# Optimization experiments

Measured on AMD Instinct MI355X. Metric: run time of the kernel, lower is better.

## Reference

```python
import jax, jax.numpy as jnp
import numpy as np

D_MODEL = 768
D_LAT = 384
N_FREQ = D_MODEL // 2 + 1  # 385
INIT_S = 0.02


def _quat_linear(x, Ww, Wx, Wy, Wz, b):
    # Ww..Wz: [out_q, in_q]; x: [..., 4*in_q]
    d = Ww.shape[1]
    xw, xx, xy, xz = x[..., :d], x[..., d:2*d], x[..., 2*d:3*d], x[..., 3*d:]
    lin = lambda W, v: jnp.einsum('...i,oi->...o', v, W)
    ow = lin(Ww, xw) - lin(Wx, xx) - lin(Wy, xy) - lin(Wz, xz)
    ox = lin(Ww, xx) + lin(Wx, xw) + lin(Wy, xz) - lin(Wz, xy)
    oy = lin(Ww, xy) - lin(Wx, xz) + lin(Wy, xw) + lin(Wz, xx)
    oz = lin(Ww, xz) + lin(Wx, xy) - lin(Wy, xx) + lin(Wz, xw)
    return jnp.concatenate([ow, ox, oy, oz], axis=-1) + b


def _filter1d(x, kr, ki, n):
    X = jnp.fft.rfft(x, axis=-1)
    K = kr + 1j * ki
    return jnp.fft.irfft(X * K, n=n, axis=-1)


def setup_inputs() -> dict:
    key = jax.random.key(0)
    ks = jax.random.split(key, 16)
    rn = lambda k, shape: jax.random.normal(k, shape, dtype=jnp.float32)
    in_q_e, out_q_e = D_MODEL // 4, D_LAT // 4   # 192, 96
    in_q_d, out_q_d = D_LAT // 4, D_MODEL // 4   # 96, 192
    return {
        'x': rn(ks[0], (8, 4096, D_MODEL)),
        'enc_kr': rn(ks[1], (N_FREQ,)) * INIT_S,
        'enc_ki': rn(ks[2], (N_FREQ,)) * INIT_S,
        'dec_kr': rn(ks[3], (N_FREQ,)) * INIT_S,
        'dec_ki': rn(ks[4], (N_FREQ,)) * INIT_S,
        'enc_Ww': rn(ks[5], (out_q_e, in_q_e)) * 0.02,
        'enc_Wx': rn(ks[6], (out_q_e, in_q_e)) * 0.02,
        'enc_Wy': rn(ks[7], (out_q_e, in_q_e)) * 0.02,
        'enc_Wz': rn(ks[8], (out_q_e, in_q_e)) * 0.02,
        'enc_b': jnp.zeros((D_LAT,), jnp.float32),
        'dec_Ww': rn(ks[9], (out_q_d, in_q_d)) * 0.02,
        'dec_Wx': rn(ks[10], (out_q_d, in_q_d)) * 0.02,
        'dec_Wy': rn(ks[11], (out_q_d, in_q_d)) * 0.02,
        'dec_Wz': rn(ks[12], (out_q_d, in_q_d)) * 0.02,
        'dec_b': jnp.zeros((D_MODEL,), jnp.float32),
    }


def reference(x, enc_kr, enc_ki, dec_kr, dec_ki,
              enc_Ww, enc_Wx, enc_Wy, enc_Wz, enc_b,
              dec_Ww, dec_Wx, dec_Wy, dec_Wz, dec_b):
    # encode: spectral filter -> GELU (exact erf, matching nn.GELU) -> quaternion proj
    h = jax.nn.gelu(_filter1d(x, enc_kr, enc_ki, D_MODEL), approximate=False)
    z = _quat_linear(h, enc_Ww, enc_Wx, enc_Wy, enc_Wz, enc_b)
    # decode: quaternion proj -> spectral filter
    recon = _filter1d(_quat_linear(z, dec_Ww, dec_Wx, dec_Wy, dec_Wz, dec_b),
                      dec_kr, dec_ki, D_MODEL)
    loss = jnp.mean((recon - jax.lax.stop_gradient(x)) ** 2)
    return z, loss
```

## Files before the change

kernel.cpp:

```cpp
#include <hip/hip_runtime.h>
#include <hip/hip_bf16.h>
#include <math.h>

typedef unsigned short u16;
typedef __attribute__((ext_vector_type(8))) short s8v;
typedef __attribute__((ext_vector_type(4))) float f4v;

#define DM 768
#define DL 384

__device__ __forceinline__ u16 f2bf(float f) {
  union { float f; unsigned u; } v; v.f = f;
  unsigned r = v.u + 0x7fffu + ((v.u >> 16) & 1u);
  return (u16)(r >> 16);
}
__device__ __forceinline__ float bf2f(u16 b) {
  union { unsigned u; float f; } v; v.u = ((unsigned)b) << 16; return v.f;
}

__global__ void k_build_c2(const float* __restrict__ kr0, const float* __restrict__ ki0,
                           const float* __restrict__ kr1, const float* __restrict__ ki1,
                           float* __restrict__ c0, float* __restrict__ c1) {
  const float* kr = blockIdx.y ? kr1 : kr0;
  const float* ki = blockIdx.y ? ki1 : ki0;
  float* c = blockIdx.y ? c1 : c0;
  const int t = blockIdx.x;
  const int f = threadIdx.x;
  float s = 0.f;
  for (int ff = f; ff < 384; ff += 256) {
    if (ff >= 1) {
      int ph = (ff * t) % DM;
      float th = (float)ph * (6.283185307179586f / DM);
      float sn, cs; sincosf(th, &sn, &cs);
      s += 2.f * (kr[ff] * cs - ki[ff] * sn);
    }
  }
  if (f == 0) s += kr[0] + ((t & 1) ? -kr[384] : kr[384]);
  __shared__ float red[256];
  red[f] = s; __syncthreads();
  for (int k = 128; k > 0; k >>= 1) {
    if (f < k) red[f] += red[f + k];
    __syncthreads();
  }
  if (f == 0) c[t] = red[0] * (1.f / DM);
}

__global__ void k_rb2(const float* __restrict__ c, const float* __restrict__ b,
                      float* __restrict__ rb) {
  const int i = blockIdx.x;
  const int f = threadIdx.x;
  float s = 0.f;
  for (int j = f; j < DM; j += 256) {
    int ci = i - j; if (ci < 0) ci += DM;
    s += c[ci] * b[j];
  }
  __shared__ float red[256];
  red[f] = s; __syncthreads();
  for (int k = 128; k > 0; k >>= 1) {
    if (f < k) red[f] += red[f + k];
    __syncthreads();
  }
  if (f == 0) rb[i] = red[0];
}

__global__ void k_circ(const float* __restrict__ c, u16* __restrict__ B) {
  int idx = blockIdx.x * 256 + threadIdx.x;
  int i = idx / DM, j = idx % DM;
  int d = i - j; if (d < 0) d += DM;
  B[idx] = f2bf(c[d]);
}

__device__ __constant__ int   MI_[4][4] = {{0,1,2,3},{1,0,3,2},{2,3,0,1},{3,2,1,0}};
__device__ __constant__ float SG_[4][4] = {{1,-1,-1,-1},{1,1,-1,1},{1,1,1,-1},{1,-1,1,1}};

__global__ void k_wenc(const float* __restrict__ Ww, const float* __restrict__ Wx,
                       const float* __restrict__ Wy, const float* __restrict__ Wz,
                       u16* __restrict__ B) {
  int idx = blockIdx.x * 256 + threadIdx.x;
  int o = idx / DM, j = idx % DM;
  int p = o / 96, r = o % 96, q = j / 192, cc = j % 192;
  const float* Ws[4] = {Ww, Wx, Wy, Wz};
  B[idx] = f2bf(SG_[p][q] * Ws[MI_[p][q]][r * 192 + cc]);
}

__global__ void k_ddecT(const float* __restrict__ Ww, const float* __restrict__ Wx,
                        const float* __restrict__ Wy, const float* __restrict__ Wz,
                        u16* __restrict__ B) {
  int idx = blockIdx.x * 256 + threadIdx.x;
  int o = idx / DM, j = idx % DM;
  int p = j / 192, r = j % 192, q = o / 96, cc = o % 96;
  const float* Ws[4] = {Ww, Wx, Wy, Wz};
  B[idx] = f2bf(SG_[p][q] * Ws[MI_[p][q]][r * 96 + cc]);
}

__global__ void k_cvt(const float4* __restrict__ x, u16* __restrict__ xb) {
  int i = blockIdx.x * 256 + threadIdx.x;
  float4 v = x[i];
  union { u16 u[4]; unsigned long long q; } o;
  o.u[0] = f2bf(v.x); o.u[1] = f2bf(v.y); o.u[2] = f2bf(v.z); o.u[3] = f2bf(v.w);
  *(unsigned long long*)(xb + (size_t)i * 4) = o.q;
}

__device__ __forceinline__ void ld_lds16(const u16* g, u16* l) {
  __builtin_amdgcn_global_load_lds((const __attribute__((address_space(1))) void*)g,
                                   (__attribute__((address_space(3))) void*)l, 16, 0, 0);
}

template <int KT, int EPI>
__global__ __launch_bounds__(512, 1) void gemm8(
    const u16* __restrict__ A, const u16* __restrict__ B,
    u16* __restrict__ outb, const float* __restrict__ bias,
    const float* __restrict__ xref, float* __restrict__ partials) {
  __shared__ __align__(16) u16 SM[65536];
  const int t = threadIdx.x;
  const int lane = t & 63, wid = t >> 6;
  const int wrow = wid >> 2, wcol = wid & 3;
  int wg = blockIdx.x;
  { const int q = gridDim.x >> 3; wg = (wg & 7) * q + (wg >> 3); }
  const int bm = wg / 3, bn = wg % 3;
  constexpr int NKT = KT / 64;

  f4v acc[8][4];
#pragma unroll
  for (int m = 0; m < 8; ++m)
#pragma unroll
    for (int n = 0; n < 4; ++n) acc[m][n] = (f4v)0.f;

  const int srow = t >> 3;
  const int sgrp = (t & 7) ^ (srow & 7);
  const u16* gA = A + (size_t)(bm * 256 + srow) * KT + sgrp * 8;
  const u16* gB = B + (size_t)(bn * 256 + srow) * KT + sgrp * 8;
  const int sx = ((lane >> 4) ^ (lane & 7)) * 8;
  const int ABASE = wrow * 8192 + (lane & 15) * 64;
  const int BBASE = 32768 + (wcol >> 1) * 8192 + (wcol & 1) * 4096 + (lane & 15) * 64;

  auto stg = [&](int opd, int kt_, int half_) {
    const u16* g = (opd ? gB : gA) + (size_t)(half_ * 128) * KT + kt_ * 64;
    u16* l = SM + opd * 32768 + (kt_ & 1) * 16384 + half_ * 8192 + t * 8;
    ld_lds16(g, l);
    ld_lds16(g + 64 * KT, l + 4096);
  };

  stg(0, 0, 0); stg(1, 0, 0); stg(0, 0, 1); stg(1, 0, 1); stg(0, 1, 0); stg(1, 1, 0);
  asm volatile("s_waitcnt vmcnt(4)" ::: "memory");
  __builtin_amdgcn_sched_barrier(0);
  __builtin_amdgcn_s_barrier();

  s8v a0[4][2], a1[4][2], b0[2][2], b1[2][2];
#pragma unroll
  for (int kt = 0; kt < NKT; ++kt) {
    const int cb = (kt & 1) * 16384;
#pragma unroll
    for (int m = 0; m < 4; ++m) {
      a0[m][0] = *(const s8v*)(SM + cb + ABASE + m * 1024 + sx);
      a0[m][1] = *(const s8v*)(SM + cb + ABASE + m * 1024 + (sx ^ 32));
    }
#pragma unroll
    for (int n = 0; n < 2; ++n) {
      b0[n][0] = *(const s8v*)(SM + cb + BBASE + n * 1024 + sx);
      b0[n][1] = *(const s8v*)(SM + cb + BBASE + n * 1024 + (sx ^ 32));
    }
    if (kt + 1 < NKT) stg(0, kt + 1, 1);
    __builtin_amdgcn_s_barrier();
    asm volatile("s_waitcnt lgkmcnt(0)" ::: "memory");
    __builtin_amdgcn_sched_barrier(0);
    __builtin_amdgcn_s_setprio(1);
#pragma unroll
    for (int m = 0; m < 4; ++m)
#pragma unroll
      for (int n = 0; n < 2; ++n) {
        acc[m][n] = __builtin_amdgcn_mfma_f32_16x16x32_bf16(a0[m][0], b0[n][0], acc[m][n], 0, 0, 0);
        acc[m][n] = __builtin_amdgcn_mfma_f32_16x16x32_bf16(a0[m][1], b0[n][1], acc[m][n], 0, 0, 0);
      }
    __builtin_amdgcn_s_setprio(0);
    __builtin_amdgcn_s_barrier();
#pragma unroll
    for (int m = 0; m < 4; ++m) {
      a1[m][0] = *(const s8v*)(SM + cb + ABASE + (4 + m) * 1024 + sx);
      a1[m][1] = *(const s8v*)(SM + cb + ABASE + (4 + m) * 1024 + (sx ^ 32));
    }
    if (kt + 1 < NKT) stg(1, kt + 1, 1);
    __builtin_amdgcn_s_barrier();
    asm volatile("s_waitcnt lgkmcnt(0)" ::: "memory");
    __builtin_amdgcn_sched_barrier(0);
    __builtin_amdgcn_s_setprio(1);
#pragma unroll
    for (int m = 0; m < 4; ++m)
#pragma unroll
      for (int n = 0; n < 2; ++n) {
        acc[4 + m][n] = __builtin_amdgcn_mfma_f32_16x16x32_bf16(a1[m][0], b0[n][0], acc[4 + m][n], 0, 0, 0);
        acc[4 + m][n] = __builtin_amdgcn_mfma_f32_16x16x32_bf16(a1[m][1], b0[n][1], acc[4 + m][n], 0, 0, 0);
      }
    __builtin_amdgcn_s_setprio(0);
    __builtin_amdgcn_s_barrier();
#pragma unroll
    for (int n = 0; n < 2; ++n) {
      b1[n][0] = *(const s8v*)(SM + cb + BBASE + (2 + n) * 1024 + sx);
      b1[n][1] = *(const s8v*)(SM + cb + BBASE + (2 + n) * 1024 + (sx ^ 32));
    }
    if (kt + 2 < NKT) stg(0, kt + 2, 0);
    __builtin_amdgcn_s_barrier();
    asm volatile("s_waitcnt lgkmcnt(0)" ::: "memory");
    __builtin_amdgcn_sched_barrier(0);
    __builtin_amdgcn_s_setprio(1);
#pragma unroll
    for (int m = 0; m < 4; ++m)
#pragma unroll
      for (int n = 0; n < 2; ++n) {
        acc[4 + m][2 + n] = __builtin_amdgcn_mfma_f32_16x16x32_bf16(a1[m][0], b1[n][0], acc[4 + m][2 + n], 0, 0, 0);
        acc[4 + m][2 + n] = __builtin_amdgcn_mfma_f32_16x16x32_bf16(a1[m][1], b1[n][1], acc[4 + m][2 + n], 0, 0, 0);
      }
    __builtin_amdgcn_s_setprio(0);
    __builtin_amdgcn_s_barrier();
    if (kt + 2 < NKT) {
      stg(1, kt + 2, 0);
      asm volatile("s_waitcnt vmcnt(4)" ::: "memory");
    } else {
      asm volatile("s_waitcnt vmcnt(0)" ::: "memory");
    }
    __builtin_amdgcn_sched_barrier(0);
    __builtin_amdgcn_s_barrier();
    __builtin_amdgcn_s_setprio(1);
#pragma unroll
    for (int m = 0; m < 4; ++m)
#pragma unroll
      for (int n = 0; n < 2; ++n) {
        acc[m][2 + n] = __builtin_amdgcn_mfma_f32_16x16x32_bf16(a0[m][0], b1[n][0], acc[m][2 + n], 0, 0, 0);
        acc[m][2 + n] = __builtin_amdgcn_mfma_f32_16x16x32_bf16(a0[m][1], b1[n][1], acc[m][2 + n], 0, 0, 0);
      }
    __builtin_amdgcn_s_setprio(0);
    __builtin_amdgcn_s_barrier();
  }

  if constexpr (EPI == 0) {
    for (int ch = 0; ch < 2; ++ch) {
      if (wrow == ch) {
#pragma unroll
        for (int m = 0; m < 8; ++m)
#pragma unroll
          for (int n = 0; n < 4; ++n)
#pragma unroll
            for (int j = 0; j < 4; ++j) {
              float v = acc[m][n][j];
              float u = v * 0.70710678118f, u2 = u * u;
              float p = u * (1.1283791671f + u2 * (-0.37612638903f +
                        u2 * (0.11283791671f + u2 * (-0.02686617064f))));
              v = 0.5f * v * (1.f + p);
              SM[(m * 16 + (lane >> 4) * 4 + j) * 264 + wcol * 64 + n * 16 + (lane & 15)] = f2bf(v);
            }
      }
      __syncthreads();
#pragma unroll
      for (int it = 0; it < 8; ++it) {
        int r = it * 16 + (t >> 5), c8 = (t & 31) * 8;
        s8v vv = *(const s8v*)(SM + r * 264 + c8);
        *(s8v*)(outb + (size_t)(bm * 256 + ch * 128 + r) * 768 + bn * 256 + c8) = vv;
      }
      __syncthreads();
    }
  } else {
    float bc[4];
#pragma unroll
    for (int n = 0; n < 4; ++n) bc[n] = bias[bn * 256 + wcol * 64 + n * 16 + (lane & 15)];
    float ls = 0.f;
#pragma unroll
    for (int m = 0; m < 8; ++m)
#pragma unroll
      for (int n = 0; n < 4; ++n)
#pragma unroll
        for (int j = 0; j < 4; ++j) {
          size_t row = bm * 256 + wrow * 128 + m * 16 + (lane >> 4) * 4 + j;
          int col = bn * 256 + wcol * 64 + n * 16 + (lane & 15);
          float v = acc[m][n][j] + bc[n];
          float d = v - xref[row * 768 + col];
          ls += d * d;
        }
#pragma unroll
    for (int o = 32; o > 0; o >>= 1) ls += __shfl_down(ls, o);
    float* rw = (float*)SM;
    if (lane == 0) rw[wid] = ls;
    __syncthreads();
    if (t == 0) {
      float s = 0.f;
#pragma unroll
      for (int i = 0; i < 8; ++i) s += rw[i];
      partials[blockIdx.x] = s;
    }
  }
}

template <int KT, int NT, int NBN, int EPI, int SWZ>
__global__ __launch_bounds__(256, 3) void gemm_bt(
    const u16* __restrict__ A, const u16* __restrict__ B,
    u16* __restrict__ outb, float* __restrict__ outf,
    const float* __restrict__ bias) {
  __shared__ __align__(16) u16 SMR[24576];
#define As_(b) (SMR + (b) * 4096)
#define Bs_(b) (SMR + 12288 + (b) * 4096)
  const int t = threadIdx.x;
  const int wid = t >> 6, lane = t & 63;
  const int wr = wid >> 1, wc = wid & 1;
  int wg = blockIdx.x;
  if (SWZ) { const int q = gridDim.x >> 3; wg = (wg & 7) * q + (wg >> 3); }
  const int bm = wg / NBN, bn = wg % NBN;

  f4v acc[4][4];
#pragma unroll
  for (int m = 0; m < 4; ++m)
#pragma unroll
    for (int n = 0; n < 4; ++n) acc[m][n] = (f4v)0.f;

  const int sgo = ((t & 3) ^ ((t >> 3) & 3)) * 8;
  const u16* gA = A + (size_t)(bm * 128 + (t >> 2)) * KT + sgo;
  const u16* gB = B + (size_t)(bn * 128 + (t >> 2)) * KT + sgo;
  const int fr = lane & 15;
  const int fo = ((lane >> 4) ^ ((fr >> 1) & 3)) * 8;
  constexpr int NK = KT / 32;

  auto stage = [&](int kt_, int b_) {
    const int ko = kt_ * 32;
    ld_lds16(gA + ko, As_(b_) + wid * 512);
    ld_lds16(gA + ko + 64 * KT, As_(b_) + wid * 512 + 2048);
    ld_lds16(gB + ko, Bs_(b_) + wid * 512);
    ld_lds16(gB + ko + 64 * KT, Bs_(b_) + wid * 512 + 2048);
  };

  stage(0, 0);
  stage(1, 1);
#pragma unroll 3
  for (int kt = 0; kt < NK; ++kt) {
    const int b0 = kt % 3, b2 = (kt + 2) % 3;
    if (kt + 2 < NK) stage(kt + 2, b2);
    const int ahead = NK - 1 - kt;
    if (ahead >= 2)      { asm volatile("s_waitcnt vmcnt(8)" ::: "memory"); }
    else if (ahead == 1) { asm volatile("s_waitcnt vmcnt(4)" ::: "memory"); }
    else                 { asm volatile("s_waitcnt vmcnt(0)" ::: "memory"); }
    __builtin_amdgcn_sched_barrier(0);
    __builtin_amdgcn_s_barrier();
    s8v af[4], bfv[4];
#pragma unroll
    for (int m = 0; m < 4; ++m)
      af[m] = *(const s8v*)(As_(b0) + (wr * 64 + m * 16 + fr) * 32 + fo);
#pragma unroll
    for (int n = 0; n < 4; ++n)
      bfv[n] = *(const s8v*)(Bs_(b0) + (wc * 64 + n * 16 + fr) * 32 + fo);
    asm volatile("s_waitcnt lgkmcnt(0)" ::: "memory");
    __builtin_amdgcn_sched_barrier(0);
    __builtin_amdgcn_s_barrier();
    __builtin_amdgcn_s_setprio(1);
#pragma unroll
    for (int m = 0; m < 4; ++m)
#pragma unroll
      for (int n = 0; n < 4; ++n)
        acc[m][n] = __builtin_amdgcn_mfma_f32_16x16x32_bf16(af[m], bfv[n], acc[m][n], 0, 0, 0);
    __builtin_amdgcn_s_setprio(0);
  }

  const int r0l = wr * 64 + ((lane >> 4) << 2);
  const int c0l = wc * 64 + (lane & 15);
  u16* Cs = SMR;
  float bc[4];
  if constexpr (EPI == 1) {
#pragma unroll
    for (int n = 0; n < 4; ++n) bc[n] = bias[bn * 128 + c0l + n * 16];
  }
#pragma unroll
  for (int m = 0; m < 4; ++m)
#pragma unroll
    for (int n = 0; n < 4; ++n)
#pragma unroll
      for (int j = 0; j < 4; ++j) {
        float v = acc[m][n][j];
        if constexpr (EPI == 1) {
          v += bc[n];
          outf[(size_t)(bm * 128 + r0l + m * 16 + j) * NT + bn * 128 + c0l + n * 16] = v;
        }
        Cs[(r0l + m * 16 + j) * 130 + c0l + n * 16] = f2bf(v);
      }
  __syncthreads();
#pragma unroll
  for (int s = 0; s < 8; ++s) {
    int idx = (s * 256 + t) * 8;
    int r = idx >> 7, c = idx & 127;
    s8v vv = *(const s8v*)(Cs + r * 130 + c);
    *(s8v*)(outb + (size_t)(bm * 128 + r) * NT + bn * 128 + c) = vv;
  }
#undef As_
#undef Bs_
}

__global__ void k_loss_final(const float* __restrict__ partials, float* __restrict__ out) {
  __shared__ float red[256];
  float s = 0.f;
  for (int i = threadIdx.x; i < 384; i += 256) s += partials[i];
  red[threadIdx.x] = s; __syncthreads();
  for (int k = 128; k > 0; k >>= 1) {
    if (threadIdx.x < k) red[threadIdx.x] += red[threadIdx.x + k];
    __syncthreads();
  }
  if (threadIdx.x == 0) out[0] = red[0] / 25165824.f;
}

extern "C" void kernel_launch(void* const* d_in, const int* in_sizes, int n_in,
                              void* d_out, int out_size, void* d_ws, size_t ws_size,
                              hipStream_t stream) {
  const float* x      = (const float*)d_in[0];
  const float* enc_kr = (const float*)d_in[1];
  const float* enc_ki = (const float*)d_in[2];
  const float* dec_kr = (const float*)d_in[3];
  const float* dec_ki = (const float*)d_in[4];
  const float* enc_Ww = (const float*)d_in[5];
  const float* enc_Wx = (const float*)d_in[6];
  const float* enc_Wy = (const float*)d_in[7];
  const float* enc_Wz = (const float*)d_in[8];
  const float* enc_b  = (const float*)d_in[9];
  const float* dec_Ww = (const float*)d_in[10];
  const float* dec_Wx = (const float*)d_in[11];
  const float* dec_Wy = (const float*)d_in[12];
  const float* dec_Wz = (const float*)d_in[13];
  const float* dec_b  = (const float*)d_in[14];

  char* ws = (char*)d_ws;
  float* c_enc    = (float*)(ws + 0);
  float* c_dec    = (float*)(ws + 4096);
  float* rb       = (float*)(ws + 8192);
  float* partials = (float*)(ws + 12288);
  u16*   Benc     = (u16*)(ws + 20480);
  u16*   Wenc     = (u16*)(ws + 1200128);
  u16*   Mdec     = (u16*)(ws + 1789952);
  u16*   Cdec     = (u16*)(ws + 2379776);
  u16*   DdT      = (u16*)(ws + 3559424);
  u16*   Xb       = (u16*)(ws + 4149248);
  u16*   Zb       = Xb;
  u16*   H        = (u16*)(ws + 54480896);

  k_build_c2<<<dim3(768, 2), 256, 0, stream>>>(enc_kr, enc_ki, dec_kr, dec_ki, c_enc, c_dec);
  k_rb2<<<768, 256, 0, stream>>>(c_dec, dec_b, rb);
  k_circ<<<2304, 256, 0, stream>>>(c_enc, Benc);
  k_circ<<<2304, 256, 0, stream>>>(c_dec, Cdec);
  k_wenc<<<1152, 256, 0, stream>>>(enc_Ww, enc_Wx, enc_Wy, enc_Wz, Wenc);
  k_ddecT<<<1152, 256, 0, stream>>>(dec_Ww, dec_Wx, dec_Wy, dec_Wz, DdT);
  gemm_bt<768, 384, 3, 3, 0><<<18, 256, 0, stream>>>(Cdec, DdT, Mdec, nullptr, nullptr);
  k_cvt<<<24576, 256, 0, stream>>>((const float4*)x, Xb);

  float* zout = (float*)d_out;
  gemm8<768, 0><<<384, 512, 0, stream>>>(Xb, Benc, H, nullptr, nullptr, nullptr);
  gemm_bt<768, 384, 3, 1, 1><<<768, 256, 0, stream>>>(H, Wenc, Zb, zout, enc_b);
  gemm8<384, 2><<<384, 512, 0, stream>>>(Zb, Mdec, nullptr, rb, x, partials);
  k_loss_final<<<1, 256, 0, stream>>>(partials, zout + (out_size - 1));
}
```

Before: 178.4 us.

## Switch big GEMMs to 256x192 tiles and route encoder projection through gemm8

The 8-wave gemm8 kernel now uses 256x192 output tiles instead of 256x256, giving 512 workgroups for the N=768 GEMMs and 256 for the N=384 encoder projection. That projection, with its bias add and fp32 z output, moves from the 4-wave gemm_bt kernel into gemm8. The two circulant-build launches are merged into one. The aim is better wave balance across CUs and use of the deeper pipelined kernel for every large GEMM, at the cost of more B reloads per A tile and a modified LDS pipeline schedule.

Measured after the change: 186.7 us. +4.7%, slower.

```diff
diff --git a/kernel.cpp b/kernel.cpp
--- a/kernel.cpp
+++ b/kernel.cpp
@@ -13,9 +13,6 @@
   union { float f; unsigned u; } v; v.f = f;
   unsigned r = v.u + 0x7fffu + ((v.u >> 16) & 1u);
   return (u16)(r >> 16);
-}
-__device__ __forceinline__ float bf2f(u16 b) {
-  union { unsigned u; float f; } v; v.u = ((unsigned)b) << 16; return v.f;
 }
 
 __global__ void k_build_c2(const float* __restrict__ kr0, const float* __restrict__ ki0,
@@ -63,7 +60,10 @@
   if (f == 0) rb[i] = red[0];
 }
 
-__global__ void k_circ(const float* __restrict__ c, u16* __restrict__ B) {
+__global__ void k_circ2(const float* __restrict__ c0, u16* __restrict__ B0,
+                        const float* __restrict__ c1, u16* __restrict__ B1) {
+  const float* c = blockIdx.y ? c1 : c0;
+  u16* B = blockIdx.y ? B1 : B0;
   int idx = blockIdx.x * 256 + threadIdx.x;
   int i = idx / DM, j = idx % DM;
   int d = i - j; if (d < 0) d += DM;
@@ -106,61 +106,68 @@
                                    (__attribute__((address_space(3))) void*)l, 16, 0, 0);
 }
 
-template <int KT, int EPI>
+template <int KT, int NT, int NBN, int EPI>
 __global__ __launch_bounds__(512, 1) void gemm8(
     const u16* __restrict__ A, const u16* __restrict__ B,
-    u16* __restrict__ outb, const float* __restrict__ bias,
-    const float* __restrict__ xref, float* __restrict__ partials) {
-  __shared__ __align__(16) u16 SM[65536];
+    u16* __restrict__ outb, float* __restrict__ outf,
+    const float* __restrict__ bias, const float* __restrict__ xref,
+    float* __restrict__ partials) {
+  __shared__ __align__(16) u16 SM[57344];
   const int t = threadIdx.x;
   const int lane = t & 63, wid = t >> 6;
   const int wrow = wid >> 2, wcol = wid & 3;
   int wg = blockIdx.x;
   { const int q = gridDim.x >> 3; wg = (wg & 7) * q + (wg >> 3); }
-  const int bm = wg / 3, bn = wg % 3;
+  const int bm = wg / NBN, bn = wg % NBN;
   constexpr int NKT = KT / 64;
 
-  f4v acc[8][4];
+  f4v acc[8][3];
 #pragma unroll
   for (int m = 0; m < 8; ++m)
 #pragma unroll
-    for (int n = 0; n < 4; ++n) acc[m][n] = (f4v)0.f;
+    for (int n = 0; n < 3; ++n) acc[m][n] = (f4v)0.f;
 
   const int srow = t >> 3;
   const int sgrp = (t & 7) ^ (srow & 7);
   const u16* gA = A + (size_t)(bm * 256 + srow) * KT + sgrp * 8;
-  const u16* gB = B + (size_t)(bn * 256 + srow) * KT + sgrp * 8;
+  const u16* gB = B + (size_t)(bn * 192 + srow) * KT + sgrp * 8;
   const int sx = ((lane >> 4) ^ (lane & 7)) * 8;
-  const int ABASE = wrow * 8192 + (lane & 15) * 64;
-  const int BBASE = 32768 + (wcol >> 1) * 8192 + (wcol & 1) * 4096 + (lane & 15) * 64;
-
-  auto stg = [&](int opd, int kt_, int half_) {
-    const u16* g = (opd ? gB : gA) + (size_t)(half_ * 128) * KT + kt_ * 64;
-    u16* l = SM + opd * 32768 + (kt_ & 1) * 16384 + half_ * 8192 + t * 8;
+  const int ar = (wrow * 128 + (lane & 15)) * 64;
+  const int br = 32768 + (wcol * 48 + (lane & 15)) * 64;
+
+  auto stgA = [&](int kt_, int half_) {
+    const u16* g = gA + (size_t)(half_ * 128) * KT + kt_ * 64;
+    u16* l = SM + (kt_ & 1) * 16384 + half_ * 8192 + t * 8;
     ld_lds16(g, l);
     ld_lds16(g + 64 * KT, l + 4096);
   };
-
-  stg(0, 0, 0); stg(1, 0, 0); stg(0, 0, 1); stg(1, 0, 1); stg(0, 1, 0); stg(1, 1, 0);
-  asm volatile("s_waitcnt vmcnt(4)" ::: "memory");
+  auto stgB = [&](int kt_, int c_) {
+    const u16* g = gB + (size_t)(c_ * 64) * KT + kt_ * 64;
+    ld_lds16(g, SM + 32768 + (kt_ & 1) * 12288 + c_ * 4096 + t * 8);
+  };
+
+  stgA(0, 0); stgA(0, 1); stgB(0, 0); stgB(0, 1); stgB(0, 2);
+  stgA(1, 0); stgB(1, 0);
+  asm volatile("s_waitcnt vmcnt(3)" ::: "memory");
   __builtin_amdgcn_sched_barrier(0);
   __builtin_amdgcn_s_barrier();
 
-  s8v a0[4][2], a1[4][2], b0[2][2], b1[2][2];
-#pragma unroll
+#pragma unroll 2
   for (int kt = 0; kt < NKT; ++kt) {
-    const int cb = (kt & 1) * 16384;
+    const int ca = (kt & 1) * 16384;
+    const int cbb = (kt & 1) * 12288;
+    s8v a0[4][2], a1[4][2], b01[2][2], b2[2];
 #pragma unroll
     for (int m = 0; m < 4; ++m) {
-      a0[m][0] = *(const s8v*)(SM + cb + ABASE + m * 1024 + sx);
-      a0[m][1] = *(const s8v*)(SM + cb + ABASE + m * 1024 + (sx ^ 32));
+      a0[m][0] = *(const s8v*)(SM + ca + ar + m * 1024 + sx);
+      a0[m][1] = *(const s8v*)(SM + ca + ar + m * 1024 + (sx ^ 32));
     }
 #pragma unroll
     for (int n = 0; n < 2; ++n) {
-      b0[n][0] = *(const s8v*)(SM + cb + BBASE + n * 1024 + sx);
-      b0[n][1] = *(const s8v*)(SM + cb + BBASE + n * 1024 + (sx ^ 32));
-    }
-    if (kt + 1 < NKT) stg(0, kt + 1, 1);
+      b01[n][0] = *(const s8v*)(SM + cbb + br + n * 1024 + sx);
+      b01[n][1] = *(const s8v*)(SM + cbb + br + n * 1024 + (sx ^ 32));
+    }
+    if (kt + 1 < NKT) stgA(kt + 1, 1);
     __builtin_amdgcn_s_barrier();
     asm volatile("s_waitcnt lgkmcnt(0)" ::: "memory");
     __builtin_amdgcn_sched_barrier(0);
@@ -169,17 +176,17 @@
     for (int m = 0; m < 4; ++m)
 #pragma unroll
       for (int n = 0; n < 2; ++n) {
-        acc[m][n] = __builtin_amdgcn_mfma_f32_16x16x32_bf16(a0[m][0], b0[n][0], acc[m][n], 0, 0, 0);
-        acc[m][n] = __builtin_amdgcn_mfma_f32_16x16x32_bf16(a0[m][1], b0[n][1], acc[m][n], 0, 0, 0);
+        acc[m][n] = __builtin_amdgcn_mfma_f32_16x16x32_bf16(a0[m][0], b01[n][0], acc[m][n], 0, 0, 0);
+        acc[m][n] = __builtin_amdgcn_mfma_f32_16x16x32_bf16(a0[m][1], b01[n][1], acc[m][n], 0, 0, 0);
       }
     __builtin_amdgcn_s_setprio(0);
     __builtin_amdgcn_s_barrier();
 #pragma unroll
     for (int m = 0; m < 4; ++m) {
-      a1[m][0] = *(const s8v*)(SM + cb + ABASE + (4 + m) * 1024 + sx);
-      a1[m][1] = *(const s8v*)(SM + cb + ABASE + (4 + m) * 1024 + (sx ^ 32));
-    }
-    if (kt + 1 < NKT) stg(1, kt + 1, 1);
+      a1[m][0] = *(const s8v*)(SM + ca + ar + (4 + m) * 1024 + sx);
+      a1[m][1] = *(const s8v*)(SM + ca + ar + (4 + m) * 1024 + (sx ^ 32));
+    }
+    if (kt + 1 < NKT) { stgB(kt + 1, 1); stgB(kt + 1, 2); }
     __builtin_amdgcn_s_barrier();
     asm volatile("s_waitcnt lgkmcnt(0)" ::: "memory");
     __builtin_amdgcn_sched_barrier(0);
@@ -188,33 +195,28 @@
     for (int m = 0; m < 4; ++m)
 #pragma unroll
       for (int n = 0; n < 2; ++n) {
-        acc[4 + m][n] = __builtin_amdgcn_mfma_f32_16x16x32_bf16(a1[m][0], b0[n][0], acc[4 + m][n], 0, 0, 0);
-        acc[4 + m][n] = __builtin_amdgcn_mfma_f32_16x16x32_bf16(a1[m][1], b0[n][1], acc[4 + m][n], 0, 0, 0);
+        acc[4 + m][n] = __builtin_amdgcn_mfma_f32_16x16x32_bf16(a1[m][0], b01[n][0], acc[4 + m][n], 0, 0, 0);
+        acc[4 + m][n] = __builtin_amdgcn_mfma_f32_16x16x32_bf16(a1[m][1], b01[n][1], acc[4 + m][n], 0, 0, 0);
       }
     __builtin_amdgcn_s_setprio(0);
     __builtin_amdgcn_s_barrier();
-#pragma unroll
-    for (int n = 0; n < 2; ++n) {
-      b1[n][0] = *(const s8v*)(SM + cb + BBASE + (2 + n) * 1024 + sx);
-      b1[n][1] = *(const s8v*)(SM + cb + BBASE + (2 + n) * 1024 + (sx ^ 32));
-    }
-    if (kt + 2 < NKT) stg(0, kt + 2, 0);
+    b2[0] = *(const s8v*)(SM + cbb + br + 2048 + sx);
+    b2[1] = *(const s8v*)(SM + cbb + br + 2048 + (sx ^ 32));
+    if (kt + 2 < NKT) stgA(kt + 2, 0);
     __builtin_amdgcn_s_barrier();
     asm volatile("s_waitcnt lgkmcnt(0)" ::: "memory");
     __builtin_amdgcn_sched_barrier(0);
     __builtin_amdgcn_s_setprio(1);
 #pragma unroll
-    for (int m = 0; m < 4; ++m)
-#pragma unroll
-      for (int n = 0; n < 2; ++n) {
-        acc[4 + m][2 + n] = __builtin_amdgcn_mfma_f32_16x16x32_bf16(a1[m][0], b1[n][0], acc[4 + m][2 + n], 0, 0, 0);
-        acc[4 + m][2 + n] = __builtin_amdgcn_mfma_f32_16x16x32_bf16(a1[m][1], b1[n][1], acc[4 + m][2 + n], 0, 0, 0);
-      }
+    for (int m = 0; m < 4; ++m) {
+      acc[4 + m][2] = __builtin_amdgcn_mfma_f32_16x16x32_bf16(a1[m][0], b2[0], acc[4 + m][2], 0, 0, 0);
+      acc[4 + m][2] = __builtin_amdgcn_mfma_f32_16x16x32_bf16(a1[m][1], b2[1], acc[4 + m][2], 0, 0, 0);
+    }
     __builtin_amdgcn_s_setprio(0);
     __builtin_amdgcn_s_barrier();
     if (kt + 2 < NKT) {
-      stg(1, kt + 2, 0);
-      asm volatile("s_waitcnt vmcnt(4)" ::: "memory");
+      stgB(kt + 2, 0);
+      asm volatile("s_waitcnt vmcnt(3)" ::: "memory");
     } else {
       asm volatile("s_waitcnt vmcnt(0)" ::: "memory");
     }
@@ -222,57 +224,29 @@
     __builtin_amdgcn_s_barrier();
     __builtin_amdgcn_s_setprio(1);
 #pragma unroll
-    for (int m = 0; m < 4; ++m)
-#pragma unroll
-      for (int n = 0; n < 2; ++n) {
-        acc[m][2 + n] = __builtin_amdgcn_mfma_f32_16x16x32_bf16(a0[m][0], b1[n][0], acc[m][2 + n], 0, 0, 0);
-        acc[m][2 + n] = __builtin_amdgcn_mfma_f32_16x16x32_bf16(a0[m][1], b1[n][1], acc[m][2 + n], 0, 0, 0);
-      }
+    for (int m = 0; m < 4; ++m) {
+      acc[m][2] = __builtin_amdgcn_mfma_f32_16x16x32_bf16(a0[m][0], b2[0], acc[m][2], 0, 0, 0);
+      acc[m][2] = __builtin_amdgcn_mfma_f32_16x16x32_bf16(a0[m][1], b2[1], acc[m][2], 0, 0, 0);
+    }
     __builtin_amdgcn_s_setprio(0);
     __builtin_amdgcn_s_barrier();
   }
 
-  if constexpr (EPI == 0) {
-    for (int ch = 0; ch < 2; ++ch) {
-      if (wrow == ch) {
-#pragma unroll
-        for (int m = 0; m < 8; ++m)
-#pragma unroll
-          for (int n = 0; n < 4; ++n)
-#pragma unroll
-            for (int j = 0; j < 4; ++j) {
-              float v = acc[m][n][j];
-              float u = v * 0.70710678118f, u2 = u * u;
-              float p = u * (1.1283791671f + u2 * (-0.37612638903f +
-                        u2 * (0.11283791671f + u2 * (-0.02686617064f))));
-              v = 0.5f * v * (1.f + p);
-              SM[(m * 16 + (lane >> 4) * 4 + j) * 264 + wcol * 64 + n * 16 + (lane & 15)] = f2bf(v);
-            }
-      }
-      __syncthreads();
-#pragma unroll
-      for (int it = 0; it < 8; ++it) {
-        int r = it * 16 + (t >> 5), c8 = (t & 31) * 8;
-        s8v vv = *(const s8v*)(SM + r * 264 + c8);
-        *(s8v*)(outb + (size_t)(bm * 256 + ch * 128 + r) * 768 + bn * 256 + c8) = vv;
-      }
-      __syncthreads();
-    }
-  } else {
-    float bc[4];
-#pragma unroll
-    for (int n = 0; n < 4; ++n) bc[n] = bias[bn * 256 + wcol * 64 + n * 16 + (lane & 15)];
+  if constexpr (EPI == 2) {
+    float bc[3];
+#pragma unroll
+    for (int n = 0; n < 3; ++n) bc[n] = bias[bn * 192 + wcol * 48 + n * 16 + (lane & 15)];
     float ls = 0.f;
 #pragma unroll
     for (int m = 0; m < 8; ++m)
 #pragma unroll
-      for (int n = 0; n < 4; ++n)
+      for (int n = 0; n < 3; ++n)
 #pragma unroll
         for (int j = 0; j < 4; ++j) {
           size_t row = bm * 256 + wrow * 128 + m * 16 + (lane >> 4) * 4 + j;
-          int col = bn * 256 + wcol * 64 + n * 16 + (lane & 15);
+          int col = bn * 192 + wcol * 48 + n * 16 + (lane & 15);
           float v = acc[m][n][j] + bc[n];
-          float d = v - xref[row * 768 + col];
+          float d = v - xref[row * NT + col];
           ls += d * d;
         }
 #pragma unroll
@@ -286,23 +260,57 @@
       for (int i = 0; i < 8; ++i) s += rw[i];
       partials[blockIdx.x] = s;
     }
-  }
-}
-
-template <int KT, int NT, int NBN, int EPI, int SWZ>
-__global__ __launch_bounds__(256, 3) void gemm_bt(
-    const u16* __restrict__ A, const u16* __restrict__ B,
-    u16* __restrict__ outb, float* __restrict__ outf,
-    const float* __restrict__ bias) {
+  } else {
+    float bc[3];
+    if constexpr (EPI == 1) {
+#pragma unroll
+      for (int n = 0; n < 3; ++n) bc[n] = bias[bn * 192 + wcol * 48 + n * 16 + (lane & 15)];
+    }
+    for (int ch = 0; ch < 2; ++ch) {
+      if (wrow == ch) {
+#pragma unroll
+        for (int m = 0; m < 8; ++m)
+#pragma unroll
+          for (int n = 0; n < 3; ++n)
+#pragma unroll
+            for (int j = 0; j < 4; ++j) {
+              float v = acc[m][n][j];
+              if constexpr (EPI == 0) {
+                float u = v * 0.70710678118f, u2 = u * u;
+                float p = u * (1.1283791671f + u2 * (-0.37612638903f +
+                          u2 * (0.11283791671f + u2 * (-0.02686617064f))));
+                v = 0.5f * v * (1.f + p);
+              } else {
+                v += bc[n];
+                outf[(size_t)(bm * 256 + ch * 128 + m * 16 + (lane >> 4) * 4 + j) * NT
+                     + bn * 192 + wcol * 48 + n * 16 + (lane & 15)] = v;
+              }
+              SM[(m * 16 + (lane >> 4) * 4 + j) * 200 + wcol * 48 + n * 16 + (lane & 15)] = f2bf(v);
+            }
+      }
+      __syncthreads();
+#pragma unroll
+      for (int it = 0; it < 6; ++it) {
+        int idx = it * 512 + t;
+        int r = idx / 24, c8 = (idx % 24) * 8;
+        s8v vv = *(const s8v*)(SM + r * 200 + c8);
+        *(s8v*)(outb + (size_t)(bm * 256 + ch * 128 + r) * NT + bn * 192 + c8) = vv;
+      }
+      __syncthreads();
+    }
+  }
+}
+
+template <int KT, int NT, int NBN>
+__global__ __launch_bounds__(256, 3) void gemm_ring(
+    const u16* __restrict__ A, const u16* __restrict__ B, u16* __restrict__ outb) {
   __shared__ __align__(16) u16 SMR[24576];
 #define As_(b) (SMR + (b) * 4096)
 #define Bs_(b) (SMR + 12288 + (b) * 4096)
   const int t = threadIdx.x;
   const int wid = t >> 6, lane = t & 63;
   const int wr = wid >> 1, wc = wid & 1;
-  int wg = blockIdx.x;
-  if (SWZ) { const int q = gridDim.x >> 3; wg = (wg & 7) * q + (wg >> 3); }
-  const int bm = wg / NBN, bn = wg % NBN;
+  const int bm = blockIdx.x / NBN, bn = blockIdx.x % NBN;
 
   f4v acc[4][4];
 #pragma unroll
@@ -359,24 +367,13 @@
   const int r0l = wr * 64 + ((lane >> 4) << 2);
   const int c0l = wc * 64 + (lane & 15);
   u16* Cs = SMR;
-  float bc[4];
-  if constexpr (EPI == 1) {
-#pragma unroll
-    for (int n = 0; n < 4; ++n) bc[n] = bias[bn * 128 + c0l + n * 16];
-  }
 #pragma unroll
   for (int m = 0; m < 4; ++m)
 #pragma unroll
     for (int n = 0; n < 4; ++n)
 #pragma unroll
-      for (int j = 0; j < 4; ++j) {
-        float v = acc[m][n][j];
-        if constexpr (EPI == 1) {
-          v += bc[n];
-          outf[(size_t)(bm * 128 + r0l + m * 16 + j) * NT + bn * 128 + c0l + n * 16] = v;
-        }
-        Cs[(r0l + m * 16 + j) * 130 + c0l + n * 16] = f2bf(v);
-      }
+      for (int j = 0; j < 4; ++j)
+        Cs[(r0l + m * 16 + j) * 130 + c0l + n * 16] = f2bf(acc[m][n][j]);
   __syncthreads();
 #pragma unroll
   for (int s = 0; s < 8; ++s) {
@@ -392,7 +389,7 @@
 __global__ void k_loss_final(const float* __restrict__ partials, float* __restrict__ out) {
   __shared__ float red[256];
   float s = 0.f;
-  for (int i = threadIdx.x; i < 384; i += 256) s += partials[i];
+  for (int i = threadIdx.x; i < 512; i += 256) s += partials[i];
   red[threadIdx.x] = s; __syncthreads();
   for (int k = 128; k > 0; k >>= 1) {
     if (threadIdx.x < k) red[threadIdx.x] += red[threadIdx.x + k];
@@ -436,16 +433,15 @@
 
   k_build_c2<<<dim3(768, 2), 256, 0, stream>>>(enc_kr, enc_ki, dec_kr, dec_ki, c_enc, c_dec);
   k_rb2<<<768, 256, 0, stream>>>(c_dec, dec_b, rb);
-  k_circ<<<2304, 256, 0, stream>>>(c_enc, Benc);
-  k_circ<<<2304, 256, 0, stream>>>(c_dec, Cdec);
+  k_circ2<<<dim3(2304, 2), 256, 0, stream>>>(c_enc, Benc, c_dec, Cdec);
   k_wenc<<<1152, 256, 0, stream>>>(enc_Ww, enc_Wx, enc_Wy, enc_Wz, Wenc);
   k_ddecT<<<1152, 256, 0, stream>>>(dec_Ww, dec_Wx, dec_Wy, dec_Wz, DdT);
-  gemm_bt<768, 384, 3, 3, 0><<<18, 256, 0, stream>>>(Cdec, DdT, Mdec, nullptr, nullptr);
+  gemm_ring<768, 384, 3><<<18, 256, 0, stream>>>(Cdec, DdT, Mdec);
   k_cvt<<<24576, 256, 0, stream>>>((const float4*)x, Xb);
 
   float* zout = (float*)d_out;
-  gemm8<768, 0><<<384, 512, 0, stream>>>(Xb, Benc, H, nullptr, nullptr, nullptr);
-  gemm_bt<768, 384, 3, 1, 1><<<768, 256, 0, stream>>>(H, Wenc, Zb, zout, enc_b);
-  gemm8<384, 2><<<384, 512, 0, stream>>>(Zb, Mdec, nullptr, rb, x, partials);
+  gemm8<768, 768, 4, 0><<<512, 512, 0, stream>>>(Xb, Benc, H, nullptr, nullptr, nullptr, nullptr);
+  gemm8<768, 384, 2, 1><<<256, 512, 0, stream>>>(H, Wenc, Zb, zout, enc_b, nullptr, nullptr);
+  gemm8<384, 768, 4, 2><<<512, 512, 0, stream>>>(Zb, Mdec, nullptr, nullptr, rb, x, partials);
   k_loss_final<<<1, 256, 0, stream>>>(partials, zout + (out_size - 1));
 }
```
